# Kernel optimization log

Hardware: AMD Instinct MI355X
Metric: run time of the kernel (lower is better)

## Reference

```python
import jax, jax.numpy as jnp
import numpy as np

B, T, IN_DIM, HID, OUT_DIM = 32, 2000, 118, 256, 118


def sru_layer(x, W, b):
    """One SRU layer. x: [B,T,n_in]; W: [n_in, k*d] with k=3 (n_in==d) or k=4; b: [2*d].
    c_t = f_t*c_{t-1} + (1-f_t)*x~_t ;  h_t = r_t*tanh(c_t) + (1-r_t)*x_hw_t
    """
    d = b.shape[0] // 2
    k = W.shape[1] // d
    U = jnp.einsum('bti,io->bto', x, W)  # [B,T,k*d] gate precompute (GEMM)
    x_tilde = U[..., :d]
    f = jax.nn.sigmoid(U[..., d:2 * d] + b[:d])
    r = jax.nn.sigmoid(U[..., 2 * d:3 * d] + b[d:])
    x_hw = U[..., 3 * d:4 * d] if k == 4 else x  # highway input (projected if dims differ)

    # elementwise recurrent scan over time (time-major)
    def step(c, ft_xt):
        ft, xt = ft_xt
        c = ft * c + (1.0 - ft) * xt
        return c, c

    f_t = jnp.swapaxes(f, 0, 1)        # [T,B,d]
    x_t = jnp.swapaxes(x_tilde, 0, 1)  # [T,B,d]
    c0 = jnp.zeros((x.shape[0], d), dtype=x.dtype)
    _, c_seq = jax.lax.scan(step, c0, (f_t, x_t))
    c = jnp.swapaxes(c_seq, 0, 1)      # [B,T,d]
    return r * jnp.tanh(c) + (1.0 - r) * x_hw


def setup_inputs() -> dict:
    key = jax.random.key(0)
    ks = jax.random.split(key, 8)
    sequence = jax.random.normal(ks[0], (B, T, IN_DIM), dtype=jnp.float32)
    lengths = jax.random.randint(ks[1], (B,), 1, T + 1)
    s0 = 1.0 / np.sqrt(IN_DIM)
    s1 = 1.0 / np.sqrt(HID)
    W0 = jax.random.uniform(ks[2], (IN_DIM, 4 * HID), jnp.float32, -s0, s0)  # k=4: n_in != n_out
    b0 = jnp.zeros((2 * HID,), jnp.float32)
    W1 = jax.random.uniform(ks[3], (HID, 3 * HID), jnp.float32, -s1, s1)    # k=3: n_in == n_out
    b1 = jnp.zeros((2 * HID,), jnp.float32)
    Wout = jax.random.uniform(ks[4], (HID, OUT_DIM), jnp.float32, -s1, s1)
    bout = jax.random.uniform(ks[5], (OUT_DIM,), jnp.float32, -s1, s1)
    return {"sequence": sequence, "lengths": lengths, "W0": W0, "b0": b0,
            "W1": W1, "b1": b1, "Wout": Wout, "bout": bout}


def reference(sequence, lengths, W0, b0, W1, b1, Wout, bout):
    h = sru_layer(sequence, W0, b0)
    h = sru_layer(h, W1, b1)
    out = jnp.einsum('btd,do->bto', h, Wout) + bout  # hidden2out Linear
    return out  # last_sigmoid=False
```

## Files before the change

### kernel.cpp

```cpp
#include <hip/hip_runtime.h>


typedef __attribute__((ext_vector_type(8))) __bf16 bf16x8;
typedef __attribute__((ext_vector_type(4))) float f32x4;
typedef __attribute__((ext_vector_type(4))) unsigned int u32x4;

static __device__ __forceinline__ float sigmoid_f(float x) {
    return 1.f / (1.f + __expf(-x));
}
static __device__ __forceinline__ float tanh_f(float x) {
    float e = __expf(-2.f * fabsf(x));
    float t = (1.f - e) / (1.f + e);
    return copysignf(t, x);
}
static __device__ __forceinline__ unsigned short f2bf(float f) {
    union { float f; unsigned u; } v; v.f = f;
    return (unsigned short)((v.u + 0x7fffu + ((v.u >> 16) & 1u)) >> 16);
}
static __device__ __forceinline__ float bf2f(unsigned short h) {
    union { unsigned u; float f; } v; v.u = ((unsigned)h) << 16;
    return v.f;
}

static constexpr int T = 2000;

__global__ void prep_x_kernel(const float* __restrict__ x, unsigned short* __restrict__ xp) {
    int i = blockIdx.x * 256 + threadIdx.x;
    if (i >= 64000 * 128) return;
    int row = i >> 7, k = i & 127;
    float v = (k < 118) ? x[row * 118 + k] : 0.f;
    xp[i] = f2bf(v);
}

__global__ void prep_w_kernel(const float* __restrict__ W0, const float* __restrict__ W1,
                              const float* __restrict__ Wout,
                              unsigned short* __restrict__ W0t, unsigned short* __restrict__ W1t,
                              unsigned short* __restrict__ Wot) {
    int i = blockIdx.x * 256 + threadIdx.x;
    if (i < 1024 * 128) {
        int n = i >> 7, k = i & 127;
        float v = (k < 118) ? W0[k * 1024 + n] : 0.f;
        W0t[i] = f2bf(v);
        return;
    }
    i -= 1024 * 128;
    if (i < 768 * 256) {
        int n = i >> 8, k = i & 255;
        W1t[i] = f2bf(W1[k * 768 + n]);
        return;
    }
    i -= 768 * 256;
    if (i < 128 * 256) {
        int n = i >> 8, k = i & 255;
        float v = (n < 118) ? Wout[k * 118 + n] : 0.f;
        Wot[i] = f2bf(v);
    }
}

template <int KP, int KFAC>
__global__ __launch_bounds__(256, 2)
void sru_layer_kernel(const unsigned short* __restrict__ xin,
                      const unsigned short* __restrict__ Wt,
                      const float* __restrict__ bvec,
                      unsigned short* __restrict__ hout) {
    constexpr int TT   = 64;
    constexpr int NTIL = (T + TT - 1) / TT;
    constexpr int KST  = KP / 32;
    constexpr int LDA  = KP + 8;
    constexpr int LDU  = TT + 4;
    constexpr int CPR  = KP / 8;
    constexpr int NLD  = TT * CPR / 256;

    __shared__ unsigned short sA[TT * LDA];
    __shared__ float sU[32 * LDU];

    const int tid  = threadIdx.x;
    const int lane = tid & 63;
    const int w    = tid >> 6;
    const int b    = blockIdx.x & 31;
    const int d0   = (blockIdx.x >> 5) * 16;

    const int nl   = lane & 15;
    const int kq   = (lane >> 4) * 8;
    const int trow = 16 * w + (lane >> 4) * 4;

    bf16x8 bfrag[KFAC][KST];
#pragma unroll
    for (int nt = 0; nt < KFAC; ++nt) {
        const unsigned short* src = Wt + (size_t)(nt * 256 + d0 + nl) * KP + kq;
#pragma unroll
        for (int ks = 0; ks < KST; ++ks)
            bfrag[nt][ks] = *(const bf16x8*)(src + ks * 32);
    }
    const float bf_r = bvec[d0 + nl];
    const float br_r = bvec[256 + d0 + nl];

    const unsigned short* xb = xin + (size_t)b * T * KP;
    unsigned short* hb = hout + (size_t)b * T * 256;

    u32x4 xreg[NLD];
    const u32x4 zero4 = {0u, 0u, 0u, 0u};
#pragma unroll
    for (int j = 0; j < NLD; ++j) {
        int idx = j * 256 + tid;
        int r = idx / CPR, cc = idx % CPR;
        xreg[j] = (r < T) ? *(const u32x4*)(xb + (size_t)r * KP + cc * 8) : zero4;
    }
#pragma unroll
    for (int j = 0; j < NLD; ++j) {
        int idx = j * 256 + tid;
        int r = idx / CPR, cc = idx % CPR;
        *(u32x4*)(&sA[r * LDA + cc * 8]) = xreg[j];
    }

    float c = 0.f;

    for (int it = 0; it < NTIL; ++it) {
        const int t0g = it * TT;
        const int ttcur = (T - t0g < TT) ? (T - t0g) : TT;

        __syncthreads();

        if (it + 1 < NTIL) {
#pragma unroll
            for (int j = 0; j < NLD; ++j) {
                int idx = j * 256 + tid;
                int r = idx / CPR, cc = idx % CPR;
                int tg = t0g + TT + r;
                xreg[j] = (tg < T) ? *(const u32x4*)(xb + (size_t)tg * KP + cc * 8) : zero4;
            }
        }

        f32x4 acc[KFAC];
        const f32x4 fz = {0.f, 0.f, 0.f, 0.f};
#pragma unroll
        for (int nt = 0; nt < KFAC; ++nt) acc[nt] = fz;
        {
            const unsigned short* arow = &sA[(16 * w + nl) * LDA + kq];
#pragma unroll
            for (int ks = 0; ks < KST; ++ks) {
                bf16x8 a = *(const bf16x8*)(arow + ks * 32);
#pragma unroll
                for (int nt = 0; nt < KFAC; ++nt)
                    acc[nt] = __builtin_amdgcn_mfma_f32_16x16x32_bf16(a, bfrag[nt][ks], acc[nt], 0, 0, 0);
            }
        }

        f32x4 fv, gv, rv;
#pragma unroll
        for (int j = 0; j < 4; ++j) {
            float f = sigmoid_f(acc[1][j] + bf_r);
            fv[j] = f;
            gv[j] = (1.f - f) * acc[0][j];
            rv[j] = sigmoid_f(acc[2][j] + br_r);
        }
        *(f32x4*)&sU[nl * LDU + trow]        = gv;
        *(f32x4*)&sU[(16 + nl) * LDU + trow] = fv;
        __syncthreads();

        if (tid < 16) {
            float cc = c;
            float* grow = &sU[tid * LDU];
            float* frow = &sU[(16 + tid) * LDU];
            for (int t4 = 0; t4 < ttcur; t4 += 4) {
                f32x4 f4 = *(f32x4*)&frow[t4];
                f32x4 g4 = *(f32x4*)&grow[t4];
                f32x4 c4;
                cc = f4.x * cc + g4.x; c4.x = cc;
                cc = f4.y * cc + g4.y; c4.y = cc;
                cc = f4.z * cc + g4.z; c4.z = cc;
                cc = f4.w * cc + g4.w; c4.w = cc;
                *(f32x4*)&grow[t4] = c4;
            }
            c = cc;
        }
        __syncthreads();

        {
            f32x4 cv = *(f32x4*)&sU[nl * LDU + trow];
#pragma unroll
            for (int j = 0; j < 4; ++j) {
                int t = trow + j;
                if (t < ttcur) {
                    float xhw;
                    if constexpr (KFAC == 4)
                        xhw = acc[3][j];
                    else
                        xhw = bf2f(xb[(size_t)(t0g + t) * KP + d0 + nl]);
                    float h = rv[j] * tanh_f(cv[j]) + (1.f - rv[j]) * xhw;
                    hb[(size_t)(t0g + t) * 256 + d0 + nl] = f2bf(h);
                }
            }
        }

        if (it + 1 < NTIL) {
#pragma unroll
            for (int j = 0; j < NLD; ++j) {
                int idx = j * 256 + tid;
                int r = idx / CPR, cc = idx % CPR;
                *(u32x4*)(&sA[r * LDA + cc * 8]) = xreg[j];
            }
        }
    }
}

__global__ __launch_bounds__(256, 2)
void out_gemm_kernel(const unsigned short* __restrict__ h1,
                     const unsigned short* __restrict__ Wt,
                     const float* __restrict__ bout,
                     float* __restrict__ out) {
    constexpr int K = 256, LDA = 264;
    const int tid = threadIdx.x, lane = tid & 63, w = tid >> 6;
    const int m0 = (blockIdx.x >> 1) * 64;
    const int n0 = (blockIdx.x & 1) * 64;

    __shared__ unsigned short sA[64 * LDA];

    bf16x8 bfrag[4][8];
    {
        const int nl = lane & 15, kq = (lane >> 4) * 8;
#pragma unroll
        for (int nt = 0; nt < 4; ++nt) {
            const unsigned short* src = Wt + (n0 + nt * 16 + nl) * K + kq;
#pragma unroll
            for (int ks = 0; ks < 8; ++ks)
                bfrag[nt][ks] = *(const bf16x8*)(src + ks * 32);
        }
    }
    {
#pragma unroll
        for (int base = 0; base < 2048; base += 256) {
            int idx = base + tid;
            int r = idx >> 5, cc = idx & 31;
            *(u32x4*)&sA[r * LDA + cc * 8] = *(const u32x4*)(h1 + (size_t)(m0 + r) * K + cc * 8);
        }
    }
    __syncthreads();

    f32x4 acc[4];
    f32x4 fz = {0.f, 0.f, 0.f, 0.f};
#pragma unroll
    for (int nt = 0; nt < 4; ++nt) acc[nt] = fz;
    {
        const unsigned short* arow = &sA[(16 * w + (lane & 15)) * LDA + (lane >> 4) * 8];
#pragma unroll
        for (int ks = 0; ks < 8; ++ks) {
            bf16x8 a = *(const bf16x8*)(arow + ks * 32);
#pragma unroll
            for (int nt = 0; nt < 4; ++nt)
                acc[nt] = __builtin_amdgcn_mfma_f32_16x16x32_bf16(a, bfrag[nt][ks], acc[nt], 0, 0, 0);
        }
    }
    {
        const int nl = lane & 15;
        const int rbase = m0 + 16 * w + (lane >> 4) * 4;
#pragma unroll
        for (int nt = 0; nt < 4; ++nt) {
            int col = n0 + nt * 16 + nl;
            if (col < 118) {
                float bo = bout[col];
#pragma unroll
                for (int j = 0; j < 4; ++j)
                    out[(size_t)(rbase + j) * 118 + col] = acc[nt][j] + bo;
            }
        }
    }
}

extern "C" void kernel_launch(void* const* d_in, const int* in_sizes, int n_in,
                              void* d_out, int out_size, void* d_ws, size_t ws_size,
                              hipStream_t stream) {
    const float* seq  = (const float*)d_in[0];
    const float* W0   = (const float*)d_in[2];
    const float* b0   = (const float*)d_in[3];
    const float* W1   = (const float*)d_in[4];
    const float* b1   = (const float*)d_in[5];
    const float* Wout = (const float*)d_in[6];
    const float* bout = (const float*)d_in[7];
    float* out = (float*)d_out;

    char* ws = (char*)d_ws;
    size_t off = 0;
    auto alloc = [&](size_t bytes) -> void* {
        void* p = ws + off;
        off = (off + bytes + 255) & ~(size_t)255;
        return p;
    };
    unsigned short* x0p = (unsigned short*)alloc(64000ull * 128 * 2);
    unsigned short* h0b = (unsigned short*)alloc(64000ull * 256 * 2);
    unsigned short* h1b = (unsigned short*)alloc(64000ull * 256 * 2);
    unsigned short* W0t = (unsigned short*)alloc(1024ull * 128 * 2);
    unsigned short* W1t = (unsigned short*)alloc(768ull * 256 * 2);
    unsigned short* Wot = (unsigned short*)alloc(128ull * 256 * 2);
    if (ws_size < off) return;

    prep_x_kernel<<<dim3(32000), dim3(256), 0, stream>>>(seq, x0p);
    prep_w_kernel<<<dim3(1408), dim3(256), 0, stream>>>(W0, W1, Wout, W0t, W1t, Wot);
    sru_layer_kernel<128, 4><<<dim3(512), dim3(256), 0, stream>>>(x0p, W0t, b0, h0b);
    sru_layer_kernel<256, 3><<<dim3(512), dim3(256), 0, stream>>>(h0b, W1t, b1, h1b);
    out_gemm_kernel<<<dim3(2000), dim3(256), 0, stream>>>(h1b, Wot, bout, out);
}
```

Measured before the change: 217.5 us.

## Replace serial per-tile time scan with parallel affine prefix scan

The linear recurrence c = f*c + g over each 64-step tile is now computed as an affine-composition prefix scan. It runs within each thread (4 steps), across lane quads via shuffles, and across the 4 waves through a small shared-memory table. Previously only 16 threads stepped through the tile serially while the rest of the block waited. The change also drops one barrier and the shared staging buffer, and hoists the highway input load ahead of the MFMA work. In exchange, more multiplies are done per element, and the hoisted highway load runs without a bounds check on the padded rows of the final tile.

New measurement: 186.7 us. 1.17x faster.

```diff
diff --git a/kernel.cpp b/kernel.cpp
--- a/kernel.cpp
+++ b/kernel.cpp
@@ -67,12 +67,11 @@
     constexpr int NTIL = (T + TT - 1) / TT;
     constexpr int KST  = KP / 32;
     constexpr int LDA  = KP + 8;
-    constexpr int LDU  = TT + 4;
     constexpr int CPR  = KP / 8;
     constexpr int NLD  = TT * CPR / 256;
 
     __shared__ unsigned short sA[TT * LDA];
-    __shared__ float sU[32 * LDU];
+    __shared__ float2 sSum[4][16];
 
     const int tid  = threadIdx.x;
     const int lane = tid & 63;
@@ -81,8 +80,9 @@
     const int d0   = (blockIdx.x >> 5) * 16;
 
     const int nl   = lane & 15;
-    const int kq   = (lane >> 4) * 8;
-    const int trow = 16 * w + (lane >> 4) * 4;
+    const int q    = lane >> 4;
+    const int kq   = q * 8;
+    const int trow = 16 * w + q * 4;
 
     bf16x8 bfrag[KFAC][KST];
 #pragma unroll
@@ -104,7 +104,7 @@
     for (int j = 0; j < NLD; ++j) {
         int idx = j * 256 + tid;
         int r = idx / CPR, cc = idx % CPR;
-        xreg[j] = (r < T) ? *(const u32x4*)(xb + (size_t)r * KP + cc * 8) : zero4;
+        xreg[j] = *(const u32x4*)(xb + (size_t)r * KP + cc * 8);
     }
 #pragma unroll
     for (int j = 0; j < NLD; ++j) {
@@ -113,7 +113,7 @@
         *(u32x4*)(&sA[r * LDA + cc * 8]) = xreg[j];
     }
 
-    float c = 0.f;
+    float c_in = 0.f;
 
     for (int it = 0; it < NTIL; ++it) {
         const int t0g = it * TT;
@@ -130,6 +130,14 @@
                 xreg[j] = (tg < T) ? *(const u32x4*)(xb + (size_t)tg * KP + cc * 8) : zero4;
             }
         }
+        unsigned short xhw_raw[4];
+        if constexpr (KFAC == 3) {
+#pragma unroll
+            for (int j = 0; j < 4; ++j) {
+                int t = trow + j;
+                xhw_raw[j] = xb[(size_t)(t0g + t) * KP + d0 + nl];
+            }
+        }
 
         f32x4 acc[KFAC];
         const f32x4 fz = {0.f, 0.f, 0.f, 0.f};
@@ -154,44 +162,55 @@
             gv[j] = (1.f - f) * acc[0][j];
             rv[j] = sigmoid_f(acc[2][j] + br_r);
         }
-        *(f32x4*)&sU[nl * LDU + trow]        = gv;
-        *(f32x4*)&sU[(16 + nl) * LDU + trow] = fv;
+
+        float F = fv[0] * fv[1];
+        float G = gv[0];
+        G = __builtin_fmaf(fv[1], G, gv[1]);
+        G = __builtin_fmaf(fv[2], G, gv[2]);
+        G = __builtin_fmaf(fv[3], G, gv[3]);
+        F = F * fv[2] * fv[3];
+
+        {
+            float Fo = __shfl_up(F, 16), Go = __shfl_up(G, 16);
+            if (q >= 1) { G = __builtin_fmaf(F, Go, G); F *= Fo; }
+            Fo = __shfl_up(F, 32); Go = __shfl_up(G, 32);
+            if (q >= 2) { G = __builtin_fmaf(F, Go, G); F *= Fo; }
+        }
+        float EF = __shfl_up(F, 16), EG = __shfl_up(G, 16);
+        if (q == 0) { EF = 1.f; EG = 0.f; }
+
+        if (q == 3) sSum[w][nl] = make_float2(F, G);
         __syncthreads();
 
-        if (tid < 16) {
-            float cc = c;
-            float* grow = &sU[tid * LDU];
-            float* frow = &sU[(16 + tid) * LDU];
-            for (int t4 = 0; t4 < ttcur; t4 += 4) {
-                f32x4 f4 = *(f32x4*)&frow[t4];
-                f32x4 g4 = *(f32x4*)&grow[t4];
-                f32x4 c4;
-                cc = f4.x * cc + g4.x; c4.x = cc;
-                cc = f4.y * cc + g4.y; c4.y = cc;
-                cc = f4.z * cc + g4.z; c4.z = cc;
-                cc = f4.w * cc + g4.w; c4.w = cc;
-                *(f32x4*)&grow[t4] = c4;
-            }
-            c = cc;
-        }
-        __syncthreads();
+        float PF = 1.f, PG = 0.f;
+        float TF = 1.f, TG = 0.f;
+#pragma unroll
+        for (int ww = 0; ww < 4; ++ww) {
+            float2 s = sSum[ww][nl];
+            if (ww < w) { PG = __builtin_fmaf(s.x, PG, s.y); PF *= s.x; }
+            TG = __builtin_fmaf(s.x, TG, s.y); TF *= s.x;
+        }
+        float cpre = __builtin_fmaf(PF, c_in, PG);
+        cpre = __builtin_fmaf(EF, cpre, EG);
 
         {
-            f32x4 cv = *(f32x4*)&sU[nl * LDU + trow];
+            float cc = cpre;
 #pragma unroll
             for (int j = 0; j < 4; ++j) {
+                cc = __builtin_fmaf(fv[j], cc, gv[j]);
                 int t = trow + j;
                 if (t < ttcur) {
                     float xhw;
                     if constexpr (KFAC == 4)
                         xhw = acc[3][j];
                     else
-                        xhw = bf2f(xb[(size_t)(t0g + t) * KP + d0 + nl]);
-                    float h = rv[j] * tanh_f(cv[j]) + (1.f - rv[j]) * xhw;
+                        xhw = bf2f(xhw_raw[j]);
+                    float h = rv[j] * tanh_f(cc) + (1.f - rv[j]) * xhw;
                     hb[(size_t)(t0g + t) * 256 + d0 + nl] = f2bf(h);
                 }
             }
         }
+        c_in = __builtin_fmaf(TF, c_in, TG);
 
         if (it + 1 < NTIL) {
 #pragma unroll
```
